# Performance work log

Hardware: AMD Instinct MI355X
Metric: run time of the kernel (lower is better)

The kernel has to match this reference:

```python
import jax, jax.numpy as jnp
import numpy as np

B, S = 512, 256          # batch, seq_len
C, H = 8, 16             # num_cells, expert hidden size
M = 20                   # memory_size (hard-coded in module)
NT = C * H               # num_trajectories = 128
ENC_IN = M * (NT + 1)    # 20*129 = 2580, memory_encode input dim
A_H = 16                 # agent LSTM hidden


def setup_inputs() -> dict:
    key = jax.random.key(0)
    ks = jax.random.split(key, 20)
    r = lambda i, shape: 0.1 * jax.random.normal(ks[i], shape, dtype=jnp.float32)
    return {
        "x": jax.random.normal(ks[0], (B, S, 1), dtype=jnp.float32),
        "pred0": jax.random.uniform(ks[1], (B, 1), dtype=jnp.float32),
        "gate0": jax.nn.softmax(jax.random.uniform(ks[2], (B, C), dtype=jnp.float32), axis=1),
        # experts: C parallel LSTM cells (input 1, hidden H) + per-cell scalar head
        "W_ih": r(3, (C, 4 * H, 1)), "W_hh": r(4, (C, 4 * H, H)),
        "b_ih": r(5, (C, 4 * H)), "b_hh": r(6, (C, 4 * H)),
        "W_o": r(7, (C, H)), "b_o": r(8, (C,)),
        # memory_encode: Linear(2580,64) ReLU Linear(64,16) ReLU
        "W1": r(9, (64, ENC_IN)), "b1": r(10, (64,)),
        "W2": r(11, (16, 64)), "b2": r(12, (16,)),
        # gate_linear: Linear(16, C) + softmax
        "Wg": r(13, (C, 16)), "bg": r(14, (C,)),
        # agent: 2 stacked LSTM cells (16 -> 16)
        "Wa_ih": r(15, (2, 4 * A_H, A_H)), "Wa_hh": r(16, (2, 4 * A_H, A_H)),
        "ba_ih": r(17, (2, 4 * A_H)), "ba_hh": r(18, (2, 4 * A_H)),
    }


def _cell(z, c):
    # PyTorch LSTMCell gate order: i, f, g, o
    i, f, g, o = jnp.split(z, 4, axis=-1)
    c2 = jax.nn.sigmoid(f) * c + jax.nn.sigmoid(i) * jnp.tanh(g)
    return jax.nn.sigmoid(o) * jnp.tanh(c2), c2


def reference(x, pred0, gate0, W_ih, W_hh, b_ih, b_hh, W_o, b_o,
              W1, b1, W2, b2, Wg, bg, Wa_ih, Wa_hh, ba_ih, ba_hh):
    mem0 = jnp.zeros((B, M, NT + 1), jnp.float32).at[:, :, -1].set(0.5)
    eh0 = jnp.zeros((B, H), jnp.float32)   # combined expert h (shared across cells)
    a0 = jnp.zeros((2, B, A_H), jnp.float32)

    def step(carry, x_t):
        mem, eh, ec, pred, gate_state, ah, ac = carry
        error = x_t - pred                                        # [B,1]
        # experts: C LSTM cells, all reading the shared combined state
        z = (jnp.einsum('bf,cgf->bcg', x_t, W_ih)
             + jnp.einsum('bh,cgh->bcg', eh, W_hh)
             + b_ih + b_hh)                                       # [B,C,4H]
        nh, nc = _cell(z, ec[:, None, :])                          # [B,C,H]
        o = jnp.einsum('bch,ch->bc', nh, W_o) + b_o               # [B,C]
        # memory_step: matmul(mstep, mem) shifts rows down by 1, row 0 <- w
        w = jnp.concatenate([nh.reshape(B, -1), error], axis=1)   # [B,NT+1]
        mem = jnp.concatenate([w[:, None, :], mem[:, :-1, :]], axis=1)
        # memory_encode MLP
        e1 = jax.nn.relu(mem.reshape(B, -1) @ W1.T + b1)
        ai = jax.nn.relu(e1 @ W2.T + b2)                           # [B,16]
        # agent: 2 stacked LSTM cells
        ah_l, ac_l, inp_l = [], [], ai
        for l in range(2):
            zl = inp_l @ Wa_ih[l].T + ba_ih[l] + ah[l] @ Wa_hh[l].T + ba_hh[l]
            hl, cl = _cell(zl, ac[l])
            ah_l.append(hl); ac_l.append(cl)
            inp_l = hl
        ah2, ac2 = jnp.stack(ah_l), jnp.stack(ac_l)
        gate = jax.nn.softmax(inp_l @ Wg.T + bg, axis=1)           # [B,C]
        # theta = clip(2.5 * mean|mem[:, :10, -1]|, 0, 1)  (relu(t)-relu(t-1))
        theta = jnp.clip(jnp.mean(jnp.abs(mem[:, :10, -1]), axis=1) * 2.5, 0.0, 1.0)[:, None]
        gate = gate * theta + gate_state * (1.0 - theta)
        eh2 = jnp.einsum('bc,bch->bh', gate, nh)                   # bmm(gate, h)
        ec2 = jnp.einsum('bc,bch->bh', gate, nc)
        pred2 = jnp.einsum('bc,bc->b', gate, o)[:, None]           # [B,1]
        return (mem, eh2, ec2, pred2, gate, ah2, ac2), pred2

    xs = jnp.swapaxes(x, 0, 1)  # [S,B,1]
    _, preds = jax.lax.scan(step, (mem0, eh0, eh0, pred0, gate0, a0, a0), xs)
    return jnp.swapaxes(preds, 0, 1)  # [B,S,1]
```

## Files before the change

### kernel.cpp

```cpp
#include <hip/hip_runtime.h>
#include <math.h>

#define S_LEN 256
#define NCELL 8
#define HID 16
#define MEM 20
#define NB 4
#define NTHR 512
#define RSTR 2592
#define RP 80

typedef _Float16 v8h __attribute__((ext_vector_type(8)));
typedef _Float16 v4h __attribute__((ext_vector_type(4)));
typedef float v4f __attribute__((ext_vector_type(4)));
typedef int v2i __attribute__((ext_vector_type(2)));
typedef int v4i __attribute__((ext_vector_type(4)));

__device__ __forceinline__ float sigm(float v) { return 1.0f / (1.0f + __expf(-v)); }
__device__ __forceinline__ float tanh_f(float v) { return 1.0f - 2.0f / (__expf(2.0f * v) + 1.0f); }
__device__ __forceinline__ float dot4(float4 a, float4 b) {
    return fmaf(a.x, b.x, fmaf(a.y, b.y, fmaf(a.z, b.z, a.w * b.w)));
}
__device__ __forceinline__ v4f mfma16(v8h a, v8h b, v4f c) {
    return __builtin_amdgcn_mfma_f32_16x16x32_f16(a, b, c, 0, 0, 0);
}
__device__ __forceinline__ int bperm(int idx4, int v) {
    return __builtin_amdgcn_ds_bpermute(idx4, v);
}

#define RING(b, s, k) ringH[(b) * RSTR + (s) * 128 + (k)]

__global__ __launch_bounds__(256)
void prep_w(const float* __restrict__ W1, const float* __restrict__ W_hh,
            const float* __restrict__ W_ih, const float* __restrict__ b_ih,
            const float* __restrict__ b_hh, const float* __restrict__ W2,
            const float* __restrict__ Wa_ih, const float* __restrict__ Wa_hh,
            _Float16* __restrict__ W1F, _Float16* __restrict__ WAF,
            _Float16* __restrict__ W2F, _Float16* __restrict__ WAGF) {
    int idx = blockIdx.x * 256 + threadIdx.x;
    if (idx < 163840) {
        int e = idx & 7, lane = (idx >> 3) & 63, jt = (idx >> 9) & 3, t = idx >> 11;
        int m = t >> 2, kc = t & 3;
        int j = jt * 16 + (lane & 15);
        int k = kc * 32 + (lane >> 4) * 8 + e;
        W1F[idx] = (_Float16)W1[j * 2580 + m * 129 + k];
    } else if (idx < 163840 + 16384) {
        int d = idx - 163840;
        int e = d & 7, lane = (d >> 3) & 63, gate = (d >> 9) & 3, c = d >> 11;
        int m = lane & 15, k = (lane >> 4) * 8 + e;
        int row = c * 64 + gate * 16 + m;
        float v = 0.f;
        if (k < 16) v = W_hh[row * 16 + k];
        else if (k == 16) v = W_ih[row];
        else if (k == 17) v = b_ih[row] + b_hh[row];
        WAF[d] = (_Float16)v;
    } else if (idx < 163840 + 16384 + 1024) {
        int d = idx - 163840 - 16384;
        int e = d & 7, lane = (d >> 3) & 63, kc = d >> 9;
        int i = lane & 15, k = kc * 32 + (lane >> 4) * 8 + e;
        W2F[d] = (_Float16)W2[i * 64 + k];
    } else if (idx < 163840 + 16384 + 1024 + 4096) {
        int d = idx - 163840 - 16384 - 1024;
        int e = d & 7, lane = (d >> 3) & 63, jt = (d >> 9) & 3, l = d >> 11;
        int g = jt * 16 + (lane & 15);
        int k = (lane >> 4) * 8 + e;
        float v = (k < 16) ? Wa_ih[(l * 64 + g) * 16 + k]
                           : Wa_hh[(l * 64 + g) * 16 + (k - 16)];
        WAGF[d] = (_Float16)v;
    }
}

#define E1P(BB, V) { \
    V = b1_l[lane] \
      + red[par][1][BB][lane] + red[par][2][BB][lane] + red[par][3][BB][lane] \
      + red[par][4][BB][lane] + red[par][5][BB][lane] + red[par][6][BB][lane] \
      + red[par][7][BB][lane]; }

__global__ __attribute__((amdgpu_flat_work_group_size(NTHR, NTHR)))
void mmoe_kernel(const float* __restrict__ x, const float* __restrict__ pred0,
                 const float* __restrict__ gate0,
                 const float* __restrict__ W_ih, const float* __restrict__ W_hh,
                 const float* __restrict__ b_ih, const float* __restrict__ b_hh,
                 const float* __restrict__ W_o, const float* __restrict__ b_o,
                 const float* __restrict__ W1, const float* __restrict__ b1,
                 const float* __restrict__ W2, const float* __restrict__ b2,
                 const float* __restrict__ Wg, const float* __restrict__ bg,
                 const float* __restrict__ Wa_ih, const float* __restrict__ Wa_hh,
                 const float* __restrict__ ba_ih, const float* __restrict__ ba_hh,
                 const _Float16* __restrict__ W1F, const _Float16* __restrict__ WAF,
                 const _Float16* __restrict__ W2F, const _Float16* __restrict__ WAGF,
                 float* __restrict__ out)
{
    __shared__ __align__(16) _Float16 ringH[NB * RSTR];
    __shared__ __align__(16) _Float16 ehH[NB][40];
    __shared__ __align__(16) _Float16 W2F_l[2 * 512];
    __shared__ __align__(16) _Float16 WaG_l[2 * 4 * 512];
    __shared__ __align__(16) _Float16 e1B[NB][64];
    __shared__ float errS[NB][MEM];
    __shared__ __align__(16) float ba_l[2][64];
    __shared__ float b2_l[16];
    __shared__ __align__(16) float Wg_l[8][16], Wo_l[8][16];
    __shared__ float bg_l[8], bo_l[8];
    __shared__ float Werr_l[MEM * 64];
    __shared__ float b1_l[64];
    __shared__ float xS[NB][S_LEN];
    __shared__ __align__(16) float ecS[NB][HID];
    __shared__ __align__(16) float nhS[NCELL][NB][HID];
    __shared__ __align__(16) float ncS[NCELL][NB][HID];
    __shared__ __align__(16) float oS[NB][NCELL];
    __shared__ float predS[NB];
    __shared__ __align__(16) float red[2][8][NB][RP];
    __shared__ __align__(16) float red0[4][NB][RP];
    __shared__ float errdotS[NB][64];
    __shared__ float thS[NB];

    const int tid = threadIdx.x;
    const int b0 = blockIdx.x * NB;
    const int lane = tid & 63, wv = tid >> 6;
    const int quad = lane >> 4, nn = lane & 15, bb4 = nn & 3;

    for (int i = tid; i < 128; i += NTHR) { int l = i >> 6, g = i & 63; ba_l[l][g] = ba_ih[i] + ba_hh[i]; }
    for (int i = tid; i < 1024; i += NTHR) W2F_l[i] = W2F[i];
    for (int i = tid; i < 4096; i += NTHR) WaG_l[i] = WAGF[i];
    for (int i = tid; i < 1280; i += NTHR) { int m = i >> 6, j = i & 63; Werr_l[i] = W1[j * 2580 + m * 129 + 128]; }
    if (tid < 64) b1_l[tid] = b1[tid];
    if (tid < 16) b2_l[tid] = b2[tid];
    if (tid < 128) { int c = tid >> 4, h = tid & 15; Wg_l[c][h] = Wg[tid]; Wo_l[c][h] = W_o[tid]; }
    if (tid < 8) { bg_l[tid] = bg[tid]; bo_l[tid] = b_o[tid]; }
    for (int i = tid; i < NB * S_LEN; i += NTHR) { int b = i >> 8, s = i & 255; xS[b][s] = x[(b0 + b) * S_LEN + s]; }
    for (int i = tid; i < NB * RSTR; i += NTHR) ringH[i] = (_Float16)0.0f;
    for (int i = tid; i < 2 * 8 * NB * RP; i += NTHR) ((float*)red)[i] = 0.0f;
    if (tid < NB * 40) {
        int n = tid / 40, k = tid % 40;
        float v = 0.f;
        if (k == 16) v = x[(b0 + n) * S_LEN + 0];
        else if (k == 17) v = 1.0f;
        ehH[n][k] = (_Float16)v;
    }
    if (tid < NB * MEM) { int b = tid / MEM, m = tid % MEM; errS[b][m] = 0.5f; }
    if (tid < NB * HID) { int b = tid >> 4, h = tid & 15; ecS[b][h] = 0.f; }
    if (tid < NB) predS[tid] = pred0[b0 + tid];

    float gS0 = gate0[(b0 + bb4) * NCELL + 0], gS1 = gate0[(b0 + bb4) * NCELL + 1];
    float gS2 = gate0[(b0 + bb4) * NCELL + 2], gS3 = gate0[(b0 + bb4) * NCELL + 3];
    float gS4 = gate0[(b0 + bb4) * NCELL + 4], gS5 = gate0[(b0 + bb4) * NCELL + 5];
    float gS6 = gate0[(b0 + bb4) * NCELL + 6], gS7 = gate0[(b0 + bb4) * NCELL + 7];
    v4f ac0 = {0.f, 0.f, 0.f, 0.f}, ac1 = {0.f, 0.f, 0.f, 0.f};
    v2i h0p = {0, 0}, h1p = {0, 0};

    const v8h* WA = (const v8h*)WAF;
    v8h aI = WA[(wv * 4 + 0) * 64 + lane];
    v8h aF = WA[(wv * 4 + 1) * 64 + lane];
    v8h aG = WA[(wv * 4 + 2) * 64 + lane];
    v8h aO = WA[(wv * 4 + 3) * 64 + lane];
    const v8h* Wb = (const v8h*)W1F;
    const int kcW = wv >> 1, jt0W = (wv & 1) * 2;
    v8h m0A = Wb[(size_t)(kcW * 4 + jt0W) * 64 + lane];
    v8h m0B = Wb[(size_t)(kcW * 4 + jt0W + 1) * 64 + lane];
    const v8h* W2Fv = (const v8h*)W2F_l;
    const v8h* WaGv = (const v8h*)WaG_l;
    __syncthreads();
    v4f b2v;
    #pragma unroll
    for (int r = 0; r < 4; ++r) b2v[r] = b2_l[quad * 4 + r];

    int head = 0;
    #pragma unroll 1
    for (int t = 0; t < S_LEN; ++t) {
        head = (head == 0) ? (MEM - 1) : (head - 1);
        const int par = t & 1, np = par ^ 1;
        float v0, v1, v2, v3;

        {
            v4f ecv = *(const v4f*)&ecS[bb4][quad * 4];
            v8h bfrag = *(const v8h*)&ehH[bb4][quad * 8];
            v4f z4 = {0.f, 0.f, 0.f, 0.f};
            v4f zi = mfma16(aI, bfrag, z4);
            v4f zf = mfma16(aF, bfrag, z4);
            v4f zg = mfma16(aG, bfrag, z4);
            v4f zo = mfma16(aO, bfrag, z4);
            v4f hv4, cv4; v4h hrS;
            #pragma unroll
            for (int r = 0; r < 4; ++r) {
                float c2 = sigm(zf[r]) * ecv[r] + sigm(zi[r]) * tanh_f(zg[r]);
                float hv = sigm(zo[r]) * tanh_f(c2);
                hv4[r] = hv; cv4[r] = c2; hrS[r] = (_Float16)hv;
            }
            if (nn < 4) {
                *(v4f*)&nhS[wv][nn][quad * 4] = hv4;
                *(v4f*)&ncS[wv][nn][quad * 4] = cv4;
                *(v4h*)&RING(nn, head, wv * 16 + quad * 4) = hrS;
            }
            if (tid < NB) errS[tid][head] = xS[tid][t] - predS[tid];
        }
        __syncthreads();

        {
            v8h bfrag = *(const v8h*)&RING(bb4, head, kcW * 32 + quad * 8);
            v4f z = {0.f, 0.f, 0.f, 0.f};
            v4f c0 = mfma16(m0A, bfrag, z);
            v4f c1 = mfma16(m0B, bfrag, z);
            if (nn < 4) {
                *(v4f*)&red0[kcW][nn][jt0W * 16 + quad * 4] = c0;
                *(v4f*)&red0[kcW][nn][(jt0W + 1) * 16 + quad * 4] = c1;
            }
            if (wv == 0) {
                E1P(0, v0) E1P(1, v1) E1P(2, v2) E1P(3, v3)
            } else if (wv == 1) {
                if (lane < 32) {
                    int bb = lane >> 3, c = lane & 7;
                    const float4* np_ = (const float4*)&nhS[c][bb][0];
                    const float4* wp = (const float4*)&Wo_l[c][0];
                    float s = bo_l[c];
                    #pragma unroll
                    for (int q4 = 0; q4 < 4; ++q4) s += dot4(np_[q4], wp[q4]);
                    oS[bb][c] = s;
                }
            } else if (wv == 2) {
                if (lane < NB) {
                    float th = 0.f;
                    #pragma unroll
                    for (int m = 0; m < 10; ++m) {
                        int sl = head + m; if (sl >= MEM) sl -= MEM;
                        th += fabsf(errS[lane][sl]);
                    }
                    th *= 0.25f;
                    thS[lane] = fminf(fmaxf(th, 0.f), 1.f);
                }
            } else if (wv >= 3 && wv < 7) {
                int bb = wv - 3;
                float s = 0.f;
                int sl = head;
                #pragma unroll
                for (int m = 0; m < MEM; ++m) {
                    s = fmaf(Werr_l[m * 64 + lane], errS[bb][sl], s);
                    ++sl; if (sl >= MEM) sl = 0;
                }
                errdotS[bb][lane] = s;
            }
        }
        __syncthreads();

        if (wv >= 1) {
            int kt = (wv - 1) * 11;
            int ktEnd = kt + 11; if (ktEnd > 76) ktEnd = 76;
            v4f c0 = {0.f,0.f,0.f,0.f}, c1 = {0.f,0.f,0.f,0.f};
            v4f c2 = {0.f,0.f,0.f,0.f}, c3 = {0.f,0.f,0.f,0.f};
            size_t tb = (size_t)(4 + kt) * 256 + lane;
            v8h pA0 = Wb[tb], pA1 = Wb[tb + 64], pA2 = Wb[tb + 128], pA3 = Wb[tb + 192];
            int m0 = 1 + (kt >> 2), kc0 = kt & 3;
            int s0 = head + m0 - 1; if (s0 >= MEM) s0 -= MEM;
            v8h pB = *(const v8h*)&RING(bb4, s0, kc0 * 32 + quad * 8);
            #pragma unroll 1
            for (; kt < ktEnd; ++kt) {
                v8h A0 = pA0, A1 = pA1, A2 = pA2, A3 = pA3, B = pB;
                int kn = kt + 1;
                if (kn < ktEnd) {
                    size_t tn = (size_t)(4 + kn) * 256 + lane;
                    pA0 = Wb[tn]; pA1 = Wb[tn + 64]; pA2 = Wb[tn + 128]; pA3 = Wb[tn + 192];
                    int mn = 1 + (kn >> 2), kcn = kn & 3;
                    int sn = head + mn - 1; if (sn >= MEM) sn -= MEM;
                    pB = *(const v8h*)&RING(bb4, sn, kcn * 32 + quad * 8);
                }
                c0 = mfma16(A0, B, c0);
                c1 = mfma16(A1, B, c1);
                c2 = mfma16(A2, B, c2);
                c3 = mfma16(A3, B, c3);
            }
            if (nn < 4) {
                *(v4f*)&red[np][wv][nn][ 0 + quad * 4] = c0;
                *(v4f*)&red[np][wv][nn][16 + quad * 4] = c1;
                *(v4f*)&red[np][wv][nn][32 + quad * 4] = c2;
                *(v4f*)&red[np][wv][nn][48 + quad * 4] = c3;
            }
        } else {
            v8h w2a = W2Fv[lane], w2b = W2Fv[64 + lane];
            v8h agA0 = WaGv[0 * 64 + lane], agA1 = WaGv[1 * 64 + lane];
            v8h agA2 = WaGv[2 * 64 + lane], agA3 = WaGv[3 * 64 + lane];
            v4f bI0 = *(const v4f*)&ba_l[0][ 0 + quad * 4];
            v4f bF0 = *(const v4f*)&ba_l[0][16 + quad * 4];
            v4f bG0 = *(const v4f*)&ba_l[0][32 + quad * 4];
            v4f bO0 = *(const v4f*)&ba_l[0][48 + quad * 4];
            float theta = thS[bb4];
            v4f oA = *(const v4f*)&oS[bb4][0], oB = *(const v4f*)&oS[bb4][4];

            {
                float r0 = fmaxf(v0 + errdotS[0][lane]
                       + red0[0][0][lane] + red0[1][0][lane] + red0[2][0][lane] + red0[3][0][lane], 0.f);
                float r1 = fmaxf(v1 + errdotS[1][lane]
                       + red0[0][1][lane] + red0[1][1][lane] + red0[2][1][lane] + red0[3][1][lane], 0.f);
                float r2 = fmaxf(v2 + errdotS[2][lane]
                       + red0[0][2][lane] + red0[1][2][lane] + red0[2][2][lane] + red0[3][2][lane], 0.f);
                float r3 = fmaxf(v3 + errdotS[3][lane]
                       + red0[0][3][lane] + red0[1][3][lane] + red0[2][3][lane] + red0[3][3][lane], 0.f);
                e1B[0][lane] = (_Float16)r0;
                e1B[1][lane] = (_Float16)r1;
                e1B[2][lane] = (_Float16)r2;
                e1B[3][lane] = (_Float16)r3;
            }
            v8h bk0 = *(const v8h*)&e1B[bb4][quad * 8];
            v8h bk1 = *(const v8h*)&e1B[bb4][32 + quad * 8];
            v4f z4 = {0.f, 0.f, 0.f, 0.f};
            v4f cai = mfma16(w2a, bk0, b2v);
            cai = mfma16(w2b, bk1, cai);
            v4h av;
            #pragma unroll
            for (int r = 0; r < 4; ++r) av[r] = (_Float16)fmaxf(cai[r], 0.f);

            const int idxA4 = (nn + ((quad & 1) << 5)) << 2;
            const int idxB4 = idxA4 + 64;
            const bool lowq = (quad < 2);

            v2i avd = __builtin_bit_cast(v2i, av);
            int tiA0 = bperm(idxA4, avd.x), tiA1 = bperm(idxA4, avd.y);
            int tiB0 = bperm(idxB4, avd.x), tiB1 = bperm(idxB4, avd.y);
            int thA0 = bperm(idxA4, h0p.x), thA1 = bperm(idxA4, h0p.y);
            int thB0 = bperm(idxB4, h0p.x), thB1 = bperm(idxB4, h0p.y);
            v4i wB0;
            wB0[0] = lowq ? tiA0 : thA0;
            wB0[1] = lowq ? tiA1 : thA1;
            wB0[2] = lowq ? tiB0 : thB0;
            wB0[3] = lowq ? tiB1 : thB1;
            v8h bf0 = __builtin_bit_cast(v8h, wB0);
            v4f zi = mfma16(agA0, bf0, z4);
            v4f zf = mfma16(agA1, bf0, z4);
            v4f zg = mfma16(agA2, bf0, z4);
            v4f zo = mfma16(agA3, bf0, z4);
            v8h agA4 = WaGv[4 * 64 + lane], agA5 = WaGv[5 * 64 + lane];
            v8h agA6 = WaGv[6 * 64 + lane], agA7 = WaGv[7 * 64 + lane];
            v4f bI1 = *(const v4f*)&ba_l[1][ 0 + quad * 4];
            v4f bF1 = *(const v4f*)&ba_l[1][16 + quad * 4];
            v4f bG1 = *(const v4f*)&ba_l[1][32 + quad * 4];
            v4f bO1 = *(const v4f*)&ba_l[1][48 + quad * 4];
            const int cbb = lane >> 4, chh = lane & 15;
            float nhp0 = nhS[0][cbb][chh], nhp1 = nhS[1][cbb][chh];
            float nhp2 = nhS[2][cbb][chh], nhp3 = nhS[3][cbb][chh];
            float nhp4 = nhS[4][cbb][chh], nhp5 = nhS[5][cbb][chh];
            float nhp6 = nhS[6][cbb][chh], nhp7 = nhS[7][cbb][chh];
            float ncp0 = ncS[0][cbb][chh], ncp1 = ncS[1][cbb][chh];
            float ncp2 = ncS[2][cbb][chh], ncp3 = ncS[3][cbb][chh];
            float ncp4 = ncS[4][cbb][chh], ncp5 = ncS[5][cbb][chh];
            float ncp6 = ncS[6][cbb][chh], ncp7 = ncS[7][cbb][chh];
            v4f wg0 = *(const v4f*)&Wg_l[0][quad * 4], wg1 = *(const v4f*)&Wg_l[1][quad * 4];
            v4f wg2 = *(const v4f*)&Wg_l[2][quad * 4], wg3 = *(const v4f*)&Wg_l[3][quad * 4];
            v4f wg4 = *(const v4f*)&Wg_l[4][quad * 4], wg5 = *(const v4f*)&Wg_l[5][quad * 4];
            v4f wg6 = *(const v4f*)&Wg_l[6][quad * 4], wg7 = *(const v4f*)&Wg_l[7][quad * 4];
            float bg0 = bg_l[0], bg1 = bg_l[1], bg2 = bg_l[2], bg3 = bg_l[3];
            float bg4 = bg_l[4], bg5 = bg_l[5], bg6 = bg_l[6], bg7 = bg_l[7];
            v4h hr0;
            #pragma unroll
            for (int r = 0; r < 4; ++r) {
                float zi_ = zi[r] + bI0[r], zf_ = zf[r] + bF0[r];
                float zg_ = zg[r] + bG0[r], zo_ = zo[r] + bO0[r];
                float c2 = sigm(zf_) * ac0[r] + sigm(zi_) * tanh_f(zg_);
                ac0[r] = c2;
                hr0[r] = (_Float16)(sigm(zo_) * tanh_f(c2));
            }
            v2i h0n = __builtin_bit_cast(v2i, hr0);

            int uiA0 = bperm(idxA4, h0n.x), uiA1 = bperm(idxA4, h0n.y);
            int uiB0 = bperm(idxB4, h0n.x), uiB1 = bperm(idxB4, h0n.y);
            int uhA0 = bperm(idxA4, h1p.x), uhA1 = bperm(idxA4, h1p.y);
            int uhB0 = bperm(idxB4, h1p.x), uhB1 = bperm(idxB4, h1p.y);
            v4i wB1;
            wB1[0] = lowq ? uiA0 : uhA0;
            wB1[1] = lowq ? uiA1 : uhA1;
            wB1[2] = lowq ? uiB0 : uhB0;
            wB1[3] = lowq ? uiB1 : uhB1;
            v8h bf1 = __builtin_bit_cast(v8h, wB1);
            v4f yi = mfma16(agA4, bf1, z4);
            v4f yf = mfma16(agA5, bf1, z4);
            v4f yg = mfma16(agA6, bf1, z4);
            v4f yo = mfma16(agA7, bf1, z4);
            h0p = h0n;
            v4h hr1; v4f hf;
            #pragma unroll
            for (int r = 0; r < 4; ++r) {
                float yi_ = yi[r] + bI1[r], yf_ = yf[r] + bF1[r];
                float yg_ = yg[r] + bG1[r], yo_ = yo[r] + bO1[r];
                float c2 = sigm(yf_) * ac1[r] + sigm(yi_) * tanh_f(yg_);
                ac1[r] = c2;
                float hv = sigm(yo_) * tanh_f(c2);
                hf[r] = hv; hr1[r] = (_Float16)hv;
            }
            h1p = __builtin_bit_cast(v2i, hr1);

            float p0 = wg0[0]*hf[0] + wg0[1]*hf[1] + wg0[2]*hf[2] + wg0[3]*hf[3];
            float p1 = wg1[0]*hf[0] + wg1[1]*hf[1] + wg1[2]*hf[2] + wg1[3]*hf[3];
            float p2 = wg2[0]*hf[0] + wg2[1]*hf[1] + wg2[2]*hf[2] + wg2[3]*hf[3];
            float p3 = wg3[0]*hf[0] + wg3[1]*hf[1] + wg3[2]*hf[2] + wg3[3]*hf[3];
            float p4 = wg4[0]*hf[0] + wg4[1]*hf[1] + wg4[2]*hf[2] + wg4[3]*hf[3];
            float p5 = wg5[0]*hf[0] + wg5[1]*hf[1] + wg5[2]*hf[2] + wg5[3]*hf[3];
            float p6 = wg6[0]*hf[0] + wg6[1]*hf[1] + wg6[2]*hf[2] + wg6[3]*hf[3];
            float p7 = wg7[0]*hf[0] + wg7[1]*hf[1] + wg7[2]*hf[2] + wg7[3]*hf[3];
            p0 += __shfl_xor(p0, 16); p0 += __shfl_xor(p0, 32);
            p1 += __shfl_xor(p1, 16); p1 += __shfl_xor(p1, 32);
            p2 += __shfl_xor(p2, 16); p2 += __shfl_xor(p2, 32);
            p3 += __shfl_xor(p3, 16); p3 += __shfl_xor(p3, 32);
            p4 += __shfl_xor(p4, 16); p4 += __shfl_xor(p4, 32);
            p5 += __shfl_xor(p5, 16); p5 += __shfl_xor(p5, 32);
            p6 += __shfl_xor(p6, 16); p6 += __shfl_xor(p6, 32);
            p7 += __shfl_xor(p7, 16); p7 += __shfl_xor(p7, 32);
            p0 += bg0; p1 += bg1; p2 += bg2; p3 += bg3;
            p4 += bg4; p5 += bg5; p6 += bg6; p7 += bg7;
            float mx = fmaxf(fmaxf(fmaxf(p0, p1), fmaxf(p2, p3)),
                             fmaxf(fmaxf(p4, p5), fmaxf(p6, p7)));
            float e0 = __expf(p0 - mx), e1 = __expf(p1 - mx), e2 = __expf(p2 - mx), e3 = __expf(p3 - mx);
            float e4 = __expf(p4 - mx), e5 = __expf(p5 - mx), e6 = __expf(p6 - mx), e7 = __expf(p7 - mx);
            float sum = ((e0 + e1) + (e2 + e3)) + ((e4 + e5) + (e6 + e7));
            float inv = 1.0f / sum;
            float omt = 1.f - theta;
            gS0 = e0 * inv * theta + gS0 * omt;
            gS1 = e1 * inv * theta + gS1 * omt;
            gS2 = e2 * inv * theta + gS2 * omt;
            gS3 = e3 * inv * theta + gS3 * omt;
            gS4 = e4 * inv * theta + gS4 * omt;
            gS5 = e5 * inv * theta + gS5 * omt;
            gS6 = e6 * inv * theta + gS6 * omt;
            gS7 = e7 * inv * theta + gS7 * omt;

            {
                const int gi = cbb << 2;
                float g0 = __int_as_float(bperm(gi, __float_as_int(gS0)));
                float g1 = __int_as_float(bperm(gi, __float_as_int(gS1)));
                float g2 = __int_as_float(bperm(gi, __float_as_int(gS2)));
                float g3 = __int_as_float(bperm(gi, __float_as_int(gS3)));
                float g4 = __int_as_float(bperm(gi, __float_as_int(gS4)));
                float g5 = __int_as_float(bperm(gi, __float_as_int(gS5)));
                float g6 = __int_as_float(bperm(gi, __float_as_int(gS6)));
                float g7 = __int_as_float(bperm(gi, __float_as_int(gS7)));
                float se = g0 * nhp0, sc = g0 * ncp0;
                se = fmaf(g1, nhp1, se); sc = fmaf(g1, ncp1, sc);
                se = fmaf(g2, nhp2, se); sc = fmaf(g2, ncp2, sc);
                se = fmaf(g3, nhp3, se); sc = fmaf(g3, ncp3, sc);
                se = fmaf(g4, nhp4, se); sc = fmaf(g4, ncp4, sc);
                se = fmaf(g5, nhp5, se); sc = fmaf(g5, ncp5, sc);
                se = fmaf(g6, nhp6, se); sc = fmaf(g6, ncp6, sc);
                se = fmaf(g7, nhp7, se); sc = fmaf(g7, ncp7, sc);
                ehH[cbb][chh] = (_Float16)se;
                ecS[cbb][chh] = sc;
            }
            if (lane < 4) {
                float s = gS0 * oA[0] + gS1 * oA[1] + gS2 * oA[2] + gS3 * oA[3]
                        + gS4 * oB[0] + gS5 * oB[1] + gS6 * oB[2] + gS7 * oB[3];
                predS[lane] = s;
                out[(b0 + lane) * S_LEN + t] = s;
                ehH[lane][16] = (_Float16)((t + 1 < S_LEN) ? xS[lane][t + 1] : 0.f);
            }
        }
        __syncthreads();
    }
}

extern "C" void kernel_launch(void* const* d_in, const int* in_sizes, int n_in,
                              void* d_out, int out_size, void* d_ws, size_t ws_size,
                              hipStream_t stream) {
    const float* xp    = (const float*)d_in[0];
    const float* pred0 = (const float*)d_in[1];
    const float* gate0 = (const float*)d_in[2];
    const float* W_ih  = (const float*)d_in[3];
    const float* W_hh  = (const float*)d_in[4];
    const float* b_ih  = (const float*)d_in[5];
    const float* b_hh  = (const float*)d_in[6];
    const float* W_o   = (const float*)d_in[7];
    const float* b_o   = (const float*)d_in[8];
    const float* W1    = (const float*)d_in[9];
    const float* b1    = (const float*)d_in[10];
    const float* W2    = (const float*)d_in[11];
    const float* b2    = (const float*)d_in[12];
    const float* Wg    = (const float*)d_in[13];
    const float* bg    = (const float*)d_in[14];
    const float* Wa_ih = (const float*)d_in[15];
    const float* Wa_hh = (const float*)d_in[16];
    const float* ba_ih = (const float*)d_in[17];
    const float* ba_hh = (const float*)d_in[18];
    _Float16* W1F  = (_Float16*)d_ws;
    _Float16* WAF  = W1F + 163840;
    _Float16* W2F  = WAF + 16384;
    _Float16* WAGF = W2F + 1024;

    prep_w<<<(163840 + 16384 + 1024 + 4096 + 255) / 256, 256, 0, stream>>>(
        W1, W_hh, W_ih, b_ih, b_hh, W2, Wa_ih, Wa_hh, W1F, WAF, W2F, WAGF);
    mmoe_kernel<<<512 / NB, NTHR, 0, stream>>>(
        xp, pred0, gate0, W_ih, W_hh, b_ih, b_hh, W_o, b_o,
        W1, b1, W2, b2, Wg, bg, Wa_ih, Wa_hh, ba_ih, ba_hh,
        W1F, WAF, W2F, WAGF, (float*)d_out);
}
```

Before: 1.270 ms.

## Remove a per-step barrier by fusing expert head and memory-encode MFMA

The first layer's contribution from the newest memory slot is moved into the later wave-group phase. That group now runs its own 16 MFMAs with weights staged in LDS and gathers the results via ds_bpermute, replacing the cross-wave red0 reduction. The per-cell output head is computed in registers with xor-shuffles right after the expert LSTM. The error for the next step is written at the end of the previous step, so one __syncthreads per timestep and the red0/predS buffers are dropped. The cost is more MFMA and permute work on the critical wave group, plus 16 KB of extra LDS, which could reduce occupancy.

```diff
diff --git a/kernel.cpp b/kernel.cpp
--- a/kernel.cpp
+++ b/kernel.cpp
@@ -26,6 +26,9 @@
 }
 __device__ __forceinline__ int bperm(int idx4, int v) {
     return __builtin_amdgcn_ds_bpermute(idx4, v);
+}
+__device__ __forceinline__ float bpermf(int idx4, float v) {
+    return __int_as_float(__builtin_amdgcn_ds_bpermute(idx4, __float_as_int(v)));
 }
 
 #define RING(b, s, k) ringH[(b) * RSTR + (s) * 128 + (k)]
@@ -95,6 +98,7 @@
     __shared__ __align__(16) _Float16 ehH[NB][40];
     __shared__ __align__(16) _Float16 W2F_l[2 * 512];
     __shared__ __align__(16) _Float16 WaG_l[2 * 4 * 512];
+    __shared__ __align__(16) _Float16 W1m0_l[8192];
     __shared__ __align__(16) _Float16 e1B[NB][64];
     __shared__ float errS[NB][MEM];
     __shared__ __align__(16) float ba_l[2][64];
@@ -108,9 +112,7 @@
     __shared__ __align__(16) float nhS[NCELL][NB][HID];
     __shared__ __align__(16) float ncS[NCELL][NB][HID];
     __shared__ __align__(16) float oS[NB][NCELL];
-    __shared__ float predS[NB];
     __shared__ __align__(16) float red[2][8][NB][RP];
-    __shared__ __align__(16) float red0[4][NB][RP];
     __shared__ float errdotS[NB][64];
     __shared__ float thS[NB];
 
@@ -122,6 +124,7 @@
     for (int i = tid; i < 128; i += NTHR) { int l = i >> 6, g = i & 63; ba_l[l][g] = ba_ih[i] + ba_hh[i]; }
     for (int i = tid; i < 1024; i += NTHR) W2F_l[i] = W2F[i];
     for (int i = tid; i < 4096; i += NTHR) WaG_l[i] = WAGF[i];
+    for (int i = tid; i < 8192; i += NTHR) W1m0_l[i] = W1F[i];
     for (int i = tid; i < 1280; i += NTHR) { int m = i >> 6, j = i & 63; Werr_l[i] = W1[j * 2580 + m * 129 + 128]; }
     if (tid < 64) b1_l[tid] = b1[tid];
     if (tid < 16) b2_l[tid] = b2[tid];
@@ -137,9 +140,11 @@
         else if (k == 17) v = 1.0f;
         ehH[n][k] = (_Float16)v;
     }
-    if (tid < NB * MEM) { int b = tid / MEM, m = tid % MEM; errS[b][m] = 0.5f; }
+    if (tid < NB * MEM) {
+        int b = tid / MEM, m = tid % MEM;
+        errS[b][m] = (m == MEM - 1) ? (x[(b0 + b) * S_LEN] - pred0[b0 + b]) : 0.5f;
+    }
     if (tid < NB * HID) { int b = tid >> 4, h = tid & 15; ecS[b][h] = 0.f; }
-    if (tid < NB) predS[tid] = pred0[b0 + tid];
 
     float gS0 = gate0[(b0 + bb4) * NCELL + 0], gS1 = gate0[(b0 + bb4) * NCELL + 1];
     float gS2 = gate0[(b0 + bb4) * NCELL + 2], gS3 = gate0[(b0 + bb4) * NCELL + 3];
@@ -154,15 +159,15 @@
     v8h aG = WA[(wv * 4 + 2) * 64 + lane];
     v8h aO = WA[(wv * 4 + 3) * 64 + lane];
     const v8h* Wb = (const v8h*)W1F;
-    const int kcW = wv >> 1, jt0W = (wv & 1) * 2;
-    v8h m0A = Wb[(size_t)(kcW * 4 + jt0W) * 64 + lane];
-    v8h m0B = Wb[(size_t)(kcW * 4 + jt0W + 1) * 64 + lane];
     const v8h* W2Fv = (const v8h*)W2F_l;
     const v8h* WaGv = (const v8h*)WaG_l;
+    const v8h* W1m0v = (const v8h*)W1m0_l;
     __syncthreads();
     v4f b2v;
     #pragma unroll
     for (int r = 0; r < 4; ++r) b2v[r] = b2_l[quad * 4 + r];
+    v4f WoR = *(const v4f*)&Wo_l[wv][quad * 4];
+    const float boR = bo_l[wv];
 
     int head = 0;
     #pragma unroll 1
@@ -186,36 +191,18 @@
                 float hv = sigm(zo[r]) * tanh_f(c2);
                 hv4[r] = hv; cv4[r] = c2; hrS[r] = (_Float16)hv;
             }
+            float op = hv4[0] * WoR[0] + hv4[1] * WoR[1] + hv4[2] * WoR[2] + hv4[3] * WoR[3];
+            op += __shfl_xor(op, 16);
+            op += __shfl_xor(op, 32);
+            op += boR;
             if (nn < 4) {
                 *(v4f*)&nhS[wv][nn][quad * 4] = hv4;
                 *(v4f*)&ncS[wv][nn][quad * 4] = cv4;
                 *(v4h*)&RING(nn, head, wv * 16 + quad * 4) = hrS;
             }
-            if (tid < NB) errS[tid][head] = xS[tid][t] - predS[tid];
-        }
-        __syncthreads();
-
-        {
-            v8h bfrag = *(const v8h*)&RING(bb4, head, kcW * 32 + quad * 8);
-            v4f z = {0.f, 0.f, 0.f, 0.f};
-            v4f c0 = mfma16(m0A, bfrag, z);
-            v4f c1 = mfma16(m0B, bfrag, z);
-            if (nn < 4) {
-                *(v4f*)&red0[kcW][nn][jt0W * 16 + quad * 4] = c0;
-                *(v4f*)&red0[kcW][nn][(jt0W + 1) * 16 + quad * 4] = c1;
-            }
+            if (lane < 4) oS[lane][wv] = op;
             if (wv == 0) {
                 E1P(0, v0) E1P(1, v1) E1P(2, v2) E1P(3, v3)
-            } else if (wv == 1) {
-                if (lane < 32) {
-                    int bb = lane >> 3, c = lane & 7;
-                    const float4* np_ = (const float4*)&nhS[c][bb][0];
-                    const float4* wp = (const float4*)&Wo_l[c][0];
-                    float s = bo_l[c];
-                    #pragma unroll
-                    for (int q4 = 0; q4 < 4; ++q4) s += dot4(np_[q4], wp[q4]);
-                    oS[bb][c] = s;
-                }
             } else if (wv == 2) {
                 if (lane < NB) {
                     float th = 0.f;
@@ -274,6 +261,16 @@
                 *(v4f*)&red[np][wv][nn][48 + quad * 4] = c3;
             }
         } else {
+            v4f z4 = {0.f, 0.f, 0.f, 0.f};
+            v4f q0 = z4, q1 = z4, q2 = z4, q3 = z4;
+            #pragma unroll
+            for (int kc = 0; kc < 4; ++kc) {
+                v8h A = *(const v8h*)&RING(bb4, head, kc * 32 + quad * 8);
+                q0 = mfma16(A, W1m0v[(kc * 4 + 0) * 64 + lane], q0);
+                q1 = mfma16(A, W1m0v[(kc * 4 + 1) * 64 + lane], q1);
+                q2 = mfma16(A, W1m0v[(kc * 4 + 2) * 64 + lane], q2);
+                q3 = mfma16(A, W1m0v[(kc * 4 + 3) * 64 + lane], q3);
+            }
             v8h w2a = W2Fv[lane], w2b = W2Fv[64 + lane];
             v8h agA0 = WaGv[0 * 64 + lane], agA1 = WaGv[1 * 64 + lane];
             v8h agA2 = WaGv[2 * 64 + lane], agA3 = WaGv[3 * 64 + lane];
@@ -284,15 +281,21 @@
             float theta = thS[bb4];
             v4f oA = *(const v4f*)&oS[bb4][0], oB = *(const v4f*)&oS[bb4][4];
 
+            const int bidx = nn << 2;
+            float t00 = bpermf(bidx, q0[0]), t01 = bpermf(bidx, q0[1]), t02 = bpermf(bidx, q0[2]), t03 = bpermf(bidx, q0[3]);
+            float t10 = bpermf(bidx, q1[0]), t11 = bpermf(bidx, q1[1]), t12 = bpermf(bidx, q1[2]), t13 = bpermf(bidx, q1[3]);
+            float t20 = bpermf(bidx, q2[0]), t21 = bpermf(bidx, q2[1]), t22 = bpermf(bidx, q2[2]), t23 = bpermf(bidx, q2[3]);
+            float t30 = bpermf(bidx, q3[0]), t31 = bpermf(bidx, q3[1]), t32 = bpermf(bidx, q3[2]), t33 = bpermf(bidx, q3[3]);
+            float m0v0 = quad == 0 ? t00 : quad == 1 ? t10 : quad == 2 ? t20 : t30;
+            float m0v1 = quad == 0 ? t01 : quad == 1 ? t11 : quad == 2 ? t21 : t31;
+            float m0v2 = quad == 0 ? t02 : quad == 1 ? t12 : quad == 2 ? t22 : t32;
+            float m0v3 = quad == 0 ? t03 : quad == 1 ? t13 : quad == 2 ? t23 : t33;
+
             {
-                float r0 = fmaxf(v0 + errdotS[0][lane]
-                       + red0[0][0][lane] + red0[1][0][lane] + red0[2][0][lane] + red0[3][0][lane], 0.f);
-                float r1 = fmaxf(v1 + errdotS[1][lane]
-                       + red0[0][1][lane] + red0[1][1][lane] + red0[2][1][lane] + red0[3][1][lane], 0.f);
-                float r2 = fmaxf(v2 + errdotS[2][lane]
-                       + red0[0][2][lane] + red0[1][2][lane] + red0[2][2][lane] + red0[3][2][lane], 0.f);
-                float r3 = fmaxf(v3 + errdotS[3][lane]
-                       + red0[0][3][lane] + red0[1][3][lane] + red0[2][3][lane] + red0[3][3][lane], 0.f);
+                float r0 = fmaxf(v0 + errdotS[0][lane] + m0v0, 0.f);
+                float r1 = fmaxf(v1 + errdotS[1][lane] + m0v1, 0.f);
+                float r2 = fmaxf(v2 + errdotS[2][lane] + m0v2, 0.f);
+                float r3 = fmaxf(v3 + errdotS[3][lane] + m0v3, 0.f);
                 e1B[0][lane] = (_Float16)r0;
                 e1B[1][lane] = (_Float16)r1;
                 e1B[2][lane] = (_Float16)r2;
@@ -300,7 +303,6 @@
             }
             v8h bk0 = *(const v8h*)&e1B[bb4][quad * 8];
             v8h bk1 = *(const v8h*)&e1B[bb4][32 + quad * 8];
-            v4f z4 = {0.f, 0.f, 0.f, 0.f};
             v4f cai = mfma16(w2a, bk0, b2v);
             cai = mfma16(w2b, bk1, cai);
             v4h av;
@@ -421,14 +423,10 @@
 
             {
                 const int gi = cbb << 2;
-                float g0 = __int_as_float(bperm(gi, __float_as_int(gS0)));
-                float g1 = __int_as_float(bperm(gi, __float_as_int(gS1)));
-                float g2 = __int_as_float(bperm(gi, __float_as_int(gS2)));
-                float g3 = __int_as_float(bperm(gi, __float_as_int(gS3)));
-                float g4 = __int_as_float(bperm(gi, __float_as_int(gS4)));
-                float g5 = __int_as_float(bperm(gi, __float_as_int(gS5)));
-                float g6 = __int_as_float(bperm(gi, __float_as_int(gS6)));
-                float g7 = __int_as_float(bperm(gi, __float_as_int(gS7)));
+                float g0 = bpermf(gi, gS0), g1 = bpermf(gi, gS1);
+                float g2 = bpermf(gi, gS2), g3 = bpermf(gi, gS3);
+                float g4 = bpermf(gi, gS4), g5 = bpermf(gi, gS5);
+                float g6 = bpermf(gi, gS6), g7 = bpermf(gi, gS7);
                 float se = g0 * nhp0, sc = g0 * ncp0;
                 se = fmaf(g1, nhp1, se); sc = fmaf(g1, ncp1, sc);
                 se = fmaf(g2, nhp2, se); sc = fmaf(g2, ncp2, sc);
@@ -443,9 +441,11 @@
             if (lane < 4) {
                 float s = gS0 * oA[0] + gS1 * oA[1] + gS2 * oA[2] + gS3 * oA[3]
                         + gS4 * oB[0] + gS5 * oB[1] + gS6 * oB[2] + gS7 * oB[3];
-                predS[lane] = s;
                 out[(b0 + lane) * S_LEN + t] = s;
-                ehH[lane][16] = (_Float16)((t + 1 < S_LEN) ? xS[lane][t + 1] : 0.f);
+                float xn = (t + 1 < S_LEN) ? xS[lane][t + 1] : 0.f;
+                int nhead = (head == 0) ? (MEM - 1) : (head - 1);
+                errS[lane][nhead] = xn - s;
+                ehH[lane][16] = (_Float16)xn;
             }
         }
         __syncthreads();
```

Result: no change. 1.278 ms (+0.6%).

## Remove per-step barrier by recomputing partner expert and exchanging via permutes

Applied to the files above, without the earlier changes.

Each wave now also computes the partner wave's expert LSTM outputs (four extra MFMAs plus activations) and assembles the first memory-encode B fragment through ds_bpermute, instead of reading the newly written ring slot after a __syncthreads. The expert output head is computed in-register with shuffles, and the theta and error-dot code use the current error directly instead of reading errS. Together these remove one block-wide barrier per timestep, at the cost of duplicated expert arithmetic and extra cross-lane traffic.

```diff
diff --git a/kernel.cpp b/kernel.cpp
--- a/kernel.cpp
+++ b/kernel.cpp
@@ -163,6 +163,8 @@
     v4f b2v;
     #pragma unroll
     for (int r = 0; r < 4; ++r) b2v[r] = b2_l[quad * 4 + r];
+    v4f WoR = *(const v4f*)&Wo_l[wv][quad * 4];
+    const float boR = bo_l[wv];
 
     int head = 0;
     #pragma unroll 1
@@ -172,6 +174,11 @@
         float v0, v1, v2, v3;
 
         {
+            const int sv = wv ^ 1;
+            v8h sI = WA[(sv * 4 + 0) * 64 + lane];
+            v8h sF = WA[(sv * 4 + 1) * 64 + lane];
+            v8h sG = WA[(sv * 4 + 2) * 64 + lane];
+            v8h sO = WA[(sv * 4 + 3) * 64 + lane];
             v4f ecv = *(const v4f*)&ecS[bb4][quad * 4];
             v8h bfrag = *(const v8h*)&ehH[bb4][quad * 8];
             v4f z4 = {0.f, 0.f, 0.f, 0.f};
@@ -191,36 +198,52 @@
                 *(v4f*)&ncS[wv][nn][quad * 4] = cv4;
                 *(v4h*)&RING(nn, head, wv * 16 + quad * 4) = hrS;
             }
+            float op = hv4[0] * WoR[0] + hv4[1] * WoR[1] + hv4[2] * WoR[2] + hv4[3] * WoR[3];
+            op += __shfl_xor(op, 16);
+            op += __shfl_xor(op, 32);
+            op += boR;
+            if (lane < 4) oS[lane][wv] = op;
+            v4f yi = mfma16(sI, bfrag, z4);
+            v4f yf = mfma16(sF, bfrag, z4);
+            v4f yg = mfma16(sG, bfrag, z4);
+            v4f yo = mfma16(sO, bfrag, z4);
+            v4h hrX;
+            #pragma unroll
+            for (int r = 0; r < 4; ++r) {
+                float c2 = sigm(yf[r]) * ecv[r] + sigm(yi[r]) * tanh_f(yg[r]);
+                hrX[r] = (_Float16)(sigm(yo[r]) * tanh_f(c2));
+            }
+            v4h hrA = (wv & 1) ? hrX : hrS;
+            v4h hrB = (wv & 1) ? hrS : hrX;
+            v2i dA = __builtin_bit_cast(v2i, hrA);
+            v2i dB = __builtin_bit_cast(v2i, hrB);
+            const int i1 = (((quad & 1) << 5) + nn) << 2;
+            const int i2 = i1 + 64;
+            int a0 = bperm(i1, dA.x), a1 = bperm(i1, dA.y);
+            int a2 = bperm(i2, dA.x), a3 = bperm(i2, dA.y);
+            int c0_ = bperm(i1, dB.x), c1_ = bperm(i1, dB.y);
+            int c2_ = bperm(i2, dB.x), c3_ = bperm(i2, dB.y);
+            const bool loq = (quad < 2);
+            v4i bmi;
+            bmi[0] = loq ? a0 : c0_;
+            bmi[1] = loq ? a1 : c1_;
+            bmi[2] = loq ? a2 : c2_;
+            bmi[3] = loq ? a3 : c3_;
+            v8h bm0 = __builtin_bit_cast(v8h, bmi);
+            v4f q0 = mfma16(m0A, bm0, z4);
+            v4f q1 = mfma16(m0B, bm0, z4);
+            if (nn < 4) {
+                *(v4f*)&red0[kcW][nn][jt0W * 16 + quad * 4] = q0;
+                *(v4f*)&red0[kcW][nn][(jt0W + 1) * 16 + quad * 4] = q1;
+            }
             if (tid < NB) errS[tid][head] = xS[tid][t] - predS[tid];
-        }
-        __syncthreads();
-
-        {
-            v8h bfrag = *(const v8h*)&RING(bb4, head, kcW * 32 + quad * 8);
-            v4f z = {0.f, 0.f, 0.f, 0.f};
-            v4f c0 = mfma16(m0A, bfrag, z);
-            v4f c1 = mfma16(m0B, bfrag, z);
-            if (nn < 4) {
-                *(v4f*)&red0[kcW][nn][jt0W * 16 + quad * 4] = c0;
-                *(v4f*)&red0[kcW][nn][(jt0W + 1) * 16 + quad * 4] = c1;
-            }
             if (wv == 0) {
                 E1P(0, v0) E1P(1, v1) E1P(2, v2) E1P(3, v3)
-            } else if (wv == 1) {
-                if (lane < 32) {
-                    int bb = lane >> 3, c = lane & 7;
-                    const float4* np_ = (const float4*)&nhS[c][bb][0];
-                    const float4* wp = (const float4*)&Wo_l[c][0];
-                    float s = bo_l[c];
-                    #pragma unroll
-                    for (int q4 = 0; q4 < 4; ++q4) s += dot4(np_[q4], wp[q4]);
-                    oS[bb][c] = s;
-                }
             } else if (wv == 2) {
                 if (lane < NB) {
-                    float th = 0.f;
+                    float th = fabsf(xS[lane][t] - predS[lane]);
                     #pragma unroll
-                    for (int m = 0; m < 10; ++m) {
+                    for (int m = 1; m < 10; ++m) {
                         int sl = head + m; if (sl >= MEM) sl -= MEM;
                         th += fabsf(errS[lane][sl]);
                     }
@@ -229,10 +252,11 @@
                 }
             } else if (wv >= 3 && wv < 7) {
                 int bb = wv - 3;
-                float s = 0.f;
-                int sl = head;
+                float err_now = xS[bb][t] - predS[bb];
+                float s = Werr_l[lane] * err_now;
+                int sl = head + 1; if (sl >= MEM) sl -= MEM;
                 #pragma unroll
-                for (int m = 0; m < MEM; ++m) {
+                for (int m = 1; m < MEM; ++m) {
                     s = fmaf(Werr_l[m * 64 + lane], errS[bb][sl], s);
                     ++sl; if (sl >= MEM) sl = 0;
                 }
```

After: 1.579 ms. 1.24x slower.
